# Optimization experiments

Hardware: AMD Instinct MI355X
Metric: run time of the kernel (lower is better)

Reference implementation:

```python
import jax, jax.numpy as jnp
import numpy as np

DIM = 768
NUM_HEADS = 12
HEAD_DIM = DIM // NUM_HEADS
SCALE = HEAD_DIM ** -0.5


def setup_inputs() -> dict:
    key = jax.random.key(0)
    ks = jax.random.split(key, 4)
    x = jax.random.normal(ks[0], (8, 1024, DIM), dtype=jnp.float32)
    # nn.Linear stores weight as [out, in]; we keep that convention.
    w_qkv = jax.random.normal(ks[1], (3 * DIM, DIM), dtype=jnp.float32) * (DIM ** -0.5)
    w_proj = jax.random.normal(ks[2], (DIM, DIM), dtype=jnp.float32) * (DIM ** -0.5)
    b_proj = jax.random.normal(ks[3], (DIM,), dtype=jnp.float32) * 0.02
    return {"x": x, "w_qkv": w_qkv, "w_proj": w_proj, "b_proj": b_proj}


def reference(x, w_qkv, w_proj, b_proj):
    B, N, C = x.shape
    H, D = NUM_HEADS, HEAD_DIM
    # qkv: [B, N, 3C] -> [3, B, H, N, D]
    qkv = jnp.einsum('bnc,oc->bno', x, w_qkv)
    qkv = qkv.reshape(B, N, 3, H, D).transpose(2, 0, 3, 1, 4)
    q, k, v = qkv[0] * SCALE, qkv[1], qkv[2]
    # attention scores [B, H, N, N]
    attn = jnp.einsum('bhnd,bhmd->bhnm', q, k)
    attn = jax.nn.softmax(attn, axis=-1)
    # weighted values -> [B, N, C]
    out = jnp.einsum('bhnm,bhmd->bhnd', attn, v)
    out = out.transpose(0, 2, 1, 3).reshape(B, N, C)
    # output projection
    return jnp.einsum('bnc,oc->bno', out, w_proj) + b_proj
```

## Files before the change

### kernel.cpp

```cpp
#include <hip/hip_runtime.h>
#include <hip/hip_bf16.h>
#include <math.h>


typedef unsigned short u16;
typedef __attribute__((ext_vector_type(8))) short bf16x8;
typedef __attribute__((ext_vector_type(4))) short bf16x4;
typedef __attribute__((ext_vector_type(4))) float f32x4;
typedef __attribute__((ext_vector_type(4))) unsigned int u32x4;

#define MFMA_BF16(a, b, c) __builtin_amdgcn_mfma_f32_16x16x32_bf16((a), (b), (c), 0, 0, 0)

#if __has_builtin(__builtin_amdgcn_mfma_f32_16x16x16bf16_1k)
#define MFMA16_BF16(a, b, c) __builtin_amdgcn_mfma_f32_16x16x16bf16_1k((a), (b), (c), 0, 0, 0)
#else
static __device__ __forceinline__ f32x4 MFMA16_BF16(bf16x4 a, bf16x4 b, f32x4 c) {
  f32x4 d;
  asm volatile("v_mfma_f32_16x16x16_bf16 %0, %1, %2, %3"
               : "=v"(d) : "v"(a), "v"(b), "v"(c));
  return d;
}
#endif

static __device__ __forceinline__ void gld_lds16(const void* g, void* l) {
  __builtin_amdgcn_global_load_lds(
      (__attribute__((address_space(1))) void*)(g),
      (__attribute__((address_space(3))) void*)(l), 16, 0, 0);
}

static __device__ __forceinline__ u16 f2bf(float f) {
  __hip_bfloat16 h = __float2bfloat16(f);
  return *(u16*)&h;
}

static __device__ __forceinline__ float fast_exp2(float x) {
#if __has_builtin(__builtin_amdgcn_exp2f)
  return __builtin_amdgcn_exp2f(x);
#else
  return exp2f(x);
#endif
}

static __device__ __forceinline__ void conv4(const float* src, u16* dst, int i) {
  const float4 v = *(const float4*)(src + i);
  float f0 = v.x, f1 = v.y, f2 = v.z, f3 = v.w;
  if (!isfinite(f0)) f0 = 0.f;
  if (!isfinite(f1)) f1 = 0.f;
  if (!isfinite(f2)) f2 = 0.f;
  if (!isfinite(f3)) f3 = 0.f;
  ushort4 o;
  o.x = f2bf(f0); o.y = f2bf(f1); o.z = f2bf(f2); o.w = f2bf(f3);
  *(ushort4*)(dst + i) = o;
}

__global__ __launch_bounds__(256) void convert3_kernel(
    const float* __restrict__ x,  u16* __restrict__ xb,
    const float* __restrict__ wq, u16* __restrict__ wqb,
    const float* __restrict__ wp, u16* __restrict__ wpb)
{
  const int blk = blockIdx.x;
  if (blk < 6144)      conv4(x,  xb,  (blk * 256 + threadIdx.x) * 4);
  else if (blk < 7872) conv4(wq, wqb, ((blk - 6144) * 256 + threadIdx.x) * 4);
  else                 conv4(wp, wpb, ((blk - 7872) * 256 + threadIdx.x) * 4);
}

__device__ __forceinline__ void gemm_tile_768(
    const u16* __restrict__ A, const u16* __restrict__ B,
    int m0, int n0, u16* ldsA, u16* ldsB, f32x4 acc[4][4])
{
  const int tid  = threadIdx.x;
  const int lane = tid & 63;
  const int wave = tid >> 6;
  const int quad = lane >> 4;
  const int l16  = lane & 15;
  const int wm = wave >> 1, wn = wave & 1;

  const u16* gA[4]; const u16* gB[4]; int ldsoff[4];
#pragma unroll
  for (int it = 0; it < 4; ++it) {
    const int c   = it * 256 + tid;
    const int row = c >> 3;
    const int cc  = (c & 7) ^ (row & 7);
    gA[it] = A + (size_t)(m0 + row) * 768 + cc * 8;
    gB[it] = B + (size_t)(n0 + row) * 768 + cc * 8;
    ldsoff[it] = (it * 256 + wave * 64) * 8;
  }

  for (int kt = 0; kt < 12; ++kt) {
    __syncthreads();
#pragma unroll
    for (int it = 0; it < 4; ++it) {
      gld_lds16(gA[it] + kt * 64, ldsA + ldsoff[it]);
      gld_lds16(gB[it] + kt * 64, ldsB + ldsoff[it]);
    }
    __syncthreads();
#pragma unroll
    for (int kc = 0; kc < 2; ++kc) {
      bf16x8 av[4], bv[4];
#pragma unroll
      for (int i = 0; i < 4; ++i) {
        const int rowA = wm * 64 + i * 16 + l16;
        av[i] = *(const bf16x8*)(ldsA + rowA * 64 + (((kc * 4 + quad) ^ (rowA & 7)) * 8));
        const int rowB = wn * 64 + i * 16 + l16;
        bv[i] = *(const bf16x8*)(ldsB + rowB * 64 + (((kc * 4 + quad) ^ (rowB & 7)) * 8));
      }
#pragma unroll
      for (int i = 0; i < 4; ++i)
#pragma unroll
        for (int j = 0; j < 4; ++j)
          acc[i][j] = MFMA_BF16(av[i], bv[j], acc[i][j]);
    }
  }
}


__global__ __launch_bounds__(256, 4) void qkv_gemm_kernel(
    const u16* __restrict__ X, const u16* __restrict__ W,
    u16* __restrict__ Qb, u16* __restrict__ Kb, u16* __restrict__ Vt)
{
  __shared__ alignas(16) u16 lds[2 * 128 * 64];
  u16* ldsA = lds;
  u16* ldsB = lds + 128 * 64;
  const int n0 = blockIdx.x * 128;
  const int m0 = blockIdx.y * 128;
  f32x4 acc[4][4];
  const f32x4 zero = {0.f, 0.f, 0.f, 0.f};
#pragma unroll
  for (int i = 0; i < 4; ++i)
#pragma unroll
    for (int j = 0; j < 4; ++j) acc[i][j] = zero;

  gemm_tile_768(X, W, m0, n0, ldsA, ldsB, acc);

  const int tid = threadIdx.x, lane = tid & 63, wave = tid >> 6;
  const int quad = lane >> 4, l16 = lane & 15;
  const int wm = wave >> 1, wn = wave & 1;

  const int which = blockIdx.x / 6;
  const bool isV = (which == 2);
  const float sc = (which == 0) ? 0.180336880f : 1.0f;
  u16* ep = lds;

  __syncthreads();
#pragma unroll
  for (int i = 0; i < 4; ++i)
#pragma unroll
    for (int j = 0; j < 4; ++j)
#pragma unroll
      for (int r = 0; r < 4; ++r) {
        const int m_l = wm * 64 + i * 16 + quad * 4 + r;
        const int o_l = wn * 64 + j * 16 + l16;
        const int row = isV ? o_l : m_l;
        const int col = isV ? m_l : o_l;
        const int ch  = col >> 3;
        const int chs = (ch & 8) | ((ch & 7) ^ (row & 7));
        ep[row * 128 + chs * 8 + (col & 7)] = f2bf(acc[i][j][r] * sc);
      }
  __syncthreads();

  const int row  = tid >> 1, half = tid & 1;
  const int b_   = m0 >> 10;
  const int nb   = m0 & 1023;
  const int oc0  = n0 - which * 768;
  u16* dst;
  if (!isV) {
    const int h = (oc0 >> 6) + half;
    dst = (which == 0 ? Qb : Kb) + (((size_t)(b_ * 12 + h)) * 1024 + nb + row) * 64;
  } else {
    const int h = (oc0 >> 6) + (row >> 6);
    const int d = row & 63;
    dst = Vt + (((size_t)(b_ * 12 + h)) * 64 + d) * 1024 + nb + half * 64;
  }
#pragma unroll
  for (int c = 0; c < 8; ++c) {
    const int chs = half * 8 + (c ^ (row & 7));
    *(u32x4*)(dst + c * 8) = *(const u32x4*)(ep + row * 128 + chs * 8);
  }
}

__global__ __launch_bounds__(256, 4) void proj_gemm_kernel(
    const u16* __restrict__ A, const u16* __restrict__ W,
    const float* __restrict__ bias, float* __restrict__ out)
{
  __shared__ alignas(16) u16 ldsA[128 * 64];
  __shared__ alignas(16) u16 ldsB[64 * 64];
  const int n0 = blockIdx.x * 64;
  const int m0 = blockIdx.y * 128;
  const int tid = threadIdx.x, lane = tid & 63, wave = tid >> 6;
  const int quad = lane >> 4, l16 = lane & 15;

  const u16* gA[4]; const u16* gB[2]; int loA[4], loB[2];
#pragma unroll
  for (int it = 0; it < 4; ++it) {
    const int c = it * 256 + tid, row = c >> 3, cc = (c & 7) ^ (row & 7);
    gA[it] = A + (size_t)(m0 + row) * 768 + cc * 8;
    loA[it] = (it * 256 + wave * 64) * 8;
  }
#pragma unroll
  for (int it = 0; it < 2; ++it) {
    const int c = it * 256 + tid, row = c >> 3, cc = (c & 7) ^ (row & 7);
    gB[it] = W + (size_t)(n0 + row) * 768 + cc * 8;
    loB[it] = (it * 256 + wave * 64) * 8;
  }

  f32x4 acc[2][4];
  const f32x4 zero = {0.f, 0.f, 0.f, 0.f};
#pragma unroll
  for (int s = 0; s < 2; ++s)
#pragma unroll
    for (int t = 0; t < 4; ++t) acc[s][t] = zero;

  for (int kt = 0; kt < 12; ++kt) {
    __syncthreads();
#pragma unroll
    for (int it = 0; it < 4; ++it) gld_lds16(gA[it] + kt * 64, ldsA + loA[it]);
#pragma unroll
    for (int it = 0; it < 2; ++it) gld_lds16(gB[it] + kt * 64, ldsB + loB[it]);
    __syncthreads();
#pragma unroll
    for (int kc = 0; kc < 2; ++kc) {
      bf16x8 av[2], bv[4];
#pragma unroll
      for (int s = 0; s < 2; ++s) {
        const int rowA = wave * 32 + s * 16 + l16;
        av[s] = *(const bf16x8*)(ldsA + rowA * 64 + (((kc * 4 + quad) ^ (rowA & 7)) * 8));
      }
#pragma unroll
      for (int t = 0; t < 4; ++t) {
        const int rowB = t * 16 + l16;
        bv[t] = *(const bf16x8*)(ldsB + rowB * 64 + (((kc * 4 + quad) ^ (rowB & 7)) * 8));
      }
#pragma unroll
      for (int s = 0; s < 2; ++s)
#pragma unroll
        for (int t = 0; t < 4; ++t)
          acc[s][t] = MFMA_BF16(av[s], bv[t], acc[s][t]);
    }
  }

  float bv4[4];
#pragma unroll
  for (int t = 0; t < 4; ++t) bv4[t] = bias[n0 + t * 16 + l16];
#pragma unroll
  for (int s = 0; s < 2; ++s)
#pragma unroll
    for (int t = 0; t < 4; ++t)
#pragma unroll
      for (int r = 0; r < 4; ++r) {
        const int m = m0 + wave * 32 + s * 16 + quad * 4 + r;
        out[(size_t)m * 768 + n0 + t * 16 + l16] = acc[s][t][r] + bv4[t];
      }
}

__global__ __launch_bounds__(256, 3) void attn_kernel(
    const u16* __restrict__ Q, const u16* __restrict__ K,
    const u16* __restrict__ Vt, __hip_bfloat16* __restrict__ O)
{
  __shared__ alignas(16) u16 ldsK[128 * 64];
  __shared__ alignas(16) u16 ldsV[64 * 128];
  const int bh = blockIdx.x;
  const int qb = blockIdx.y;
  const int tid = threadIdx.x;
  const int wave = tid >> 6, lane = tid & 63;
  const int quad = lane >> 4, l16 = lane & 15;

  const int q0 = qb * 128 + wave * 32;
  const u16* Kbh = K  + (size_t)bh * (1024 * 64);
  const u16* Vbh = Vt + (size_t)bh * (64 * 1024);

  const u16* gK[4]; const u16* gV[4]; int lo[4];
#pragma unroll
  for (int it = 0; it < 4; ++it) {
    const int c = it * 256 + tid;
    {
      const int row = c >> 3, cc = (c & 7) ^ (row & 7);
      gK[it] = Kbh + (size_t)row * 64 + cc * 8;
    }
    {
      const int row = c >> 4, slot = c & 15;
      const int cc = (slot & 8) | ((slot & 7) ^ (row & 7));
      gV[it] = Vbh + (size_t)row * 1024 + cc * 8;
    }
    lo[it] = (it * 256 + wave * 64) * 8;
  }

  bf16x8 aQ0[2], aQ1[2];
#pragma unroll
  for (int s = 0; s < 2; ++s) {
    const u16* qp = Q + ((size_t)bh * 1024 + q0 + s * 16 + l16) * 64 + quad * 8;
    aQ0[s] = *(const bf16x8*)qp;
    aQ1[s] = *(const bf16x8*)(qp + 32);
  }

  f32x4 oacc[2][4];
  const f32x4 zero = {0.f, 0.f, 0.f, 0.f};
#pragma unroll
  for (int s = 0; s < 2; ++s)
#pragma unroll
    for (int db = 0; db < 4; ++db) oacc[s][db] = zero;
  float lacc[2] = {0.f, 0.f};

  for (int kt = 0; kt < 8; ++kt) {
    __syncthreads();
#pragma unroll
    for (int it = 0; it < 4; ++it) {
      gld_lds16(gK[it] + (size_t)kt * 128 * 64, ldsK + lo[it]);
      gld_lds16(gV[it] + kt * 128, ldsV + lo[it]);
    }
    __syncthreads();

#pragma unroll
    for (int ph = 0; ph < 2; ++ph) {
      bf16x8 kb0[4], kb1[4];
#pragma unroll
      for (int t = 0; t < 4; ++t) {
        const int row = ph * 64 + t * 16 + l16;
        kb0[t] = *(const bf16x8*)(ldsK + row * 64 + (((0 * 4 + quad) ^ (row & 7)) * 8));
        kb1[t] = *(const bf16x8*)(ldsK + row * 64 + (((1 * 4 + quad) ^ (row & 7)) * 8));
      }
      bf16x4 pa[2][4];
#pragma unroll
      for (int s = 0; s < 2; ++s) {
#pragma unroll
        for (int t = 0; t < 4; ++t) {
          f32x4 z = zero;
          z = MFMA_BF16(kb0[t], aQ0[s], z);
          z = MFMA_BF16(kb1[t], aQ1[s], z);
          const float p0 = fast_exp2(z[0]);
          const float p1 = fast_exp2(z[1]);
          const float p2 = fast_exp2(z[2]);
          const float p3 = fast_exp2(z[3]);
          lacc[s] += (p0 + p1) + (p2 + p3);
          bf16x4 pk;
          pk[0] = (short)f2bf(p0); pk[1] = (short)f2bf(p1);
          pk[2] = (short)f2bf(p2); pk[3] = (short)f2bf(p3);
          pa[s][t] = pk;
        }
      }
#pragma unroll
      for (int db = 0; db < 4; ++db) {
        const int d = db * 16 + l16;
#pragma unroll
        for (int t = 0; t < 4; ++t) {
          const int slot = ph * 8 + ((t * 2 + (quad >> 1)) ^ (d & 7));
          const bf16x4 v = *(const bf16x4*)(ldsV + d * 128 + slot * 8 + (quad & 1) * 4);
#pragma unroll
          for (int s = 0; s < 2; ++s)
            oacc[s][db] = MFMA16_BF16(pa[s][t], v, oacc[s][db]);
        }
      }
    }
  }

  const int b = bh / 12, h = bh - (bh / 12) * 12;
  float linv[2];
#pragma unroll
  for (int s = 0; s < 2; ++s) {
    float l = lacc[s];
    l += __shfl_xor(l, 16);
    l += __shfl_xor(l, 32);
    linv[s] = 1.f / l;
  }
#pragma unroll
  for (int s = 0; s < 2; ++s) {
#pragma unroll
    for (int r = 0; r < 4; ++r) {
      const float inv = __shfl(linv[s], quad * 4 + r);
      const int n = q0 + s * 16 + quad * 4 + r;
      __hip_bfloat16* orow = O + ((size_t)b * 1024 + n) * 768 + h * 64;
#pragma unroll
      for (int db = 0; db < 4; ++db)
        orow[db * 16 + l16] = __float2bfloat16(oacc[s][db][r] * inv);
    }
  }
}

extern "C" void kernel_launch(void* const* d_in, const int* in_sizes, int n_in,
                              void* d_out, int out_size, void* d_ws, size_t ws_size,
                              hipStream_t stream) {
  const float* x      = (const float*)d_in[0];
  const float* w_qkv  = (const float*)d_in[1];
  const float* w_proj = (const float*)d_in[2];
  const float* b_proj = (const float*)d_in[3];
  float* out = (float*)d_out;

  char* ws = (char*)d_ws;
  const size_t SEG = (size_t)96 * 1024 * 64 * sizeof(u16);
  u16* xb   = (u16*)(ws + 0 * SEG);
  u16* Qb   = (u16*)(ws + 1 * SEG);
  u16* Kb   = (u16*)(ws + 2 * SEG);
  u16* AO   = (u16*)(ws + 3 * SEG);
  u16* Vt   = (u16*)(ws + 4 * SEG);
  u16* wqb  = (u16*)(ws + 5 * SEG);
  u16* wpb  = (u16*)(ws + 5 * SEG + 3538944);

  convert3_kernel<<<8448, 256, 0, stream>>>(x, xb, w_qkv, wqb, w_proj, wpb);
  qkv_gemm_kernel<<<dim3(18, 64), 256, 0, stream>>>(xb, wqb, Qb, Kb, Vt);
  attn_kernel    <<<dim3(96, 8), 256, 0, stream>>>(Qb, Kb, Vt, (__hip_bfloat16*)AO);
  proj_gemm_kernel<<<dim3(12, 64), 256, 0, stream>>>(AO, wpb, b_proj, out);
}
```

Measured before the change: 201.7 us.

## Split QKV GEMM and attention tiles across 8 waves per block

Both the QKV projection GEMM and the attention kernel now launch 512 threads (8 waves) per block while keeping the same tile sizes, so each wave owns half the previous work: a 64x32 sub-tile in the GEMM and 16 query rows in attention. Global-to-LDS loads are spread over more threads, and the QKV epilogue write-out is reindexed for four threads per row. The aim is more waves in flight to hide latency and lower register pressure per wave. In exchange, LDS fragment reuse per wave drops (K/V fragments are read from LDS twice as often relative to MFMA work), and synchronisation now covers more waves.

```diff
diff --git a/kernel.cpp b/kernel.cpp
--- a/kernel.cpp
+++ b/kernel.cpp
@@ -64,57 +64,8 @@
   else                 conv4(wp, wpb, ((blk - 7872) * 256 + threadIdx.x) * 4);
 }
 
-__device__ __forceinline__ void gemm_tile_768(
-    const u16* __restrict__ A, const u16* __restrict__ B,
-    int m0, int n0, u16* ldsA, u16* ldsB, f32x4 acc[4][4])
-{
-  const int tid  = threadIdx.x;
-  const int lane = tid & 63;
-  const int wave = tid >> 6;
-  const int quad = lane >> 4;
-  const int l16  = lane & 15;
-  const int wm = wave >> 1, wn = wave & 1;
-
-  const u16* gA[4]; const u16* gB[4]; int ldsoff[4];
-#pragma unroll
-  for (int it = 0; it < 4; ++it) {
-    const int c   = it * 256 + tid;
-    const int row = c >> 3;
-    const int cc  = (c & 7) ^ (row & 7);
-    gA[it] = A + (size_t)(m0 + row) * 768 + cc * 8;
-    gB[it] = B + (size_t)(n0 + row) * 768 + cc * 8;
-    ldsoff[it] = (it * 256 + wave * 64) * 8;
-  }
-
-  for (int kt = 0; kt < 12; ++kt) {
-    __syncthreads();
-#pragma unroll
-    for (int it = 0; it < 4; ++it) {
-      gld_lds16(gA[it] + kt * 64, ldsA + ldsoff[it]);
-      gld_lds16(gB[it] + kt * 64, ldsB + ldsoff[it]);
-    }
-    __syncthreads();
-#pragma unroll
-    for (int kc = 0; kc < 2; ++kc) {
-      bf16x8 av[4], bv[4];
-#pragma unroll
-      for (int i = 0; i < 4; ++i) {
-        const int rowA = wm * 64 + i * 16 + l16;
-        av[i] = *(const bf16x8*)(ldsA + rowA * 64 + (((kc * 4 + quad) ^ (rowA & 7)) * 8));
-        const int rowB = wn * 64 + i * 16 + l16;
-        bv[i] = *(const bf16x8*)(ldsB + rowB * 64 + (((kc * 4 + quad) ^ (rowB & 7)) * 8));
-      }
-#pragma unroll
-      for (int i = 0; i < 4; ++i)
-#pragma unroll
-        for (int j = 0; j < 4; ++j)
-          acc[i][j] = MFMA_BF16(av[i], bv[j], acc[i][j]);
-    }
-  }
-}
-
-
-__global__ __launch_bounds__(256, 4) void qkv_gemm_kernel(
+
+__global__ __launch_bounds__(512, 4) void qkv_gemm_kernel(
     const u16* __restrict__ X, const u16* __restrict__ W,
     u16* __restrict__ Qb, u16* __restrict__ Kb, u16* __restrict__ Vt)
 {
@@ -123,18 +74,56 @@
   u16* ldsB = lds + 128 * 64;
   const int n0 = blockIdx.x * 128;
   const int m0 = blockIdx.y * 128;
-  f32x4 acc[4][4];
-  const f32x4 zero = {0.f, 0.f, 0.f, 0.f};
-#pragma unroll
-  for (int i = 0; i < 4; ++i)
-#pragma unroll
-    for (int j = 0; j < 4; ++j) acc[i][j] = zero;
-
-  gemm_tile_768(X, W, m0, n0, ldsA, ldsB, acc);
-
   const int tid = threadIdx.x, lane = tid & 63, wave = tid >> 6;
   const int quad = lane >> 4, l16 = lane & 15;
-  const int wm = wave >> 1, wn = wave & 1;
+  const int wm = wave >> 2, wn = wave & 3;
+
+  const u16* gA[2]; const u16* gB[2]; int lo[2];
+#pragma unroll
+  for (int it = 0; it < 2; ++it) {
+    const int c = it * 512 + tid;
+    const int row = c >> 3;
+    const int cc  = (c & 7) ^ (row & 7);
+    gA[it] = X + (size_t)(m0 + row) * 768 + cc * 8;
+    gB[it] = W + (size_t)(n0 + row) * 768 + cc * 8;
+    lo[it] = (it * 512 + wave * 64) * 8;
+  }
+
+  f32x4 acc[4][2];
+  const f32x4 zero = {0.f, 0.f, 0.f, 0.f};
+#pragma unroll
+  for (int i = 0; i < 4; ++i)
+#pragma unroll
+    for (int j = 0; j < 2; ++j) acc[i][j] = zero;
+
+  for (int kt = 0; kt < 12; ++kt) {
+    __syncthreads();
+#pragma unroll
+    for (int it = 0; it < 2; ++it) {
+      gld_lds16(gA[it] + kt * 64, ldsA + lo[it]);
+      gld_lds16(gB[it] + kt * 64, ldsB + lo[it]);
+    }
+    __syncthreads();
+#pragma unroll
+    for (int kc = 0; kc < 2; ++kc) {
+      bf16x8 av[4], bv[2];
+#pragma unroll
+      for (int i = 0; i < 4; ++i) {
+        const int rowA = wm * 64 + i * 16 + l16;
+        av[i] = *(const bf16x8*)(ldsA + rowA * 64 + (((kc * 4 + quad) ^ (rowA & 7)) * 8));
+      }
+#pragma unroll
+      for (int j = 0; j < 2; ++j) {
+        const int rowB = wn * 32 + j * 16 + l16;
+        bv[j] = *(const bf16x8*)(ldsB + rowB * 64 + (((kc * 4 + quad) ^ (rowB & 7)) * 8));
+      }
+#pragma unroll
+      for (int i = 0; i < 4; ++i)
+#pragma unroll
+        for (int j = 0; j < 2; ++j)
+          acc[i][j] = MFMA_BF16(av[i], bv[j], acc[i][j]);
+    }
+  }
 
   const int which = blockIdx.x / 6;
   const bool isV = (which == 2);
@@ -145,11 +134,11 @@
 #pragma unroll
   for (int i = 0; i < 4; ++i)
 #pragma unroll
-    for (int j = 0; j < 4; ++j)
+    for (int j = 0; j < 2; ++j)
 #pragma unroll
       for (int r = 0; r < 4; ++r) {
         const int m_l = wm * 64 + i * 16 + quad * 4 + r;
-        const int o_l = wn * 64 + j * 16 + l16;
+        const int o_l = wn * 32 + j * 16 + l16;
         const int row = isV ? o_l : m_l;
         const int col = isV ? m_l : o_l;
         const int ch  = col >> 3;
@@ -158,23 +147,26 @@
       }
   __syncthreads();
 
-  const int row  = tid >> 1, half = tid & 1;
-  const int b_   = m0 >> 10;
-  const int nb   = m0 & 1023;
-  const int oc0  = n0 - which * 768;
-  u16* dst;
-  if (!isV) {
-    const int h = (oc0 >> 6) + half;
-    dst = (which == 0 ? Qb : Kb) + (((size_t)(b_ * 12 + h)) * 1024 + nb + row) * 64;
-  } else {
-    const int h = (oc0 >> 6) + (row >> 6);
-    const int d = row & 63;
-    dst = Vt + (((size_t)(b_ * 12 + h)) * 64 + d) * 1024 + nb + half * 64;
-  }
-#pragma unroll
-  for (int c = 0; c < 8; ++c) {
-    const int chs = half * 8 + (c ^ (row & 7));
-    *(u32x4*)(dst + c * 8) = *(const u32x4*)(ep + row * 128 + chs * 8);
+  const int row = tid >> 2, qtr = tid & 3;
+  const int b_  = m0 >> 10;
+  const int nb  = m0 & 1023;
+  const int oc0 = n0 - which * 768;
+#pragma unroll
+  for (int c = 0; c < 4; ++c) {
+    const int ch  = qtr * 4 + c;
+    const int chs = (ch & 8) | ((ch & 7) ^ (row & 7));
+    const u32x4 val = *(const u32x4*)(ep + row * 128 + chs * 8);
+    if (!isV) {
+      const int feat = ch * 8;
+      const int h = (oc0 >> 6) + (feat >> 6), d = feat & 63;
+      u16* dst = (which == 0 ? Qb : Kb) +
+                 (((size_t)(b_ * 12 + h)) * 1024 + nb + row) * 64 + d;
+      *(u32x4*)dst = val;
+    } else {
+      const int h = (oc0 >> 6) + (row >> 6), d = row & 63;
+      u16* dst = Vt + (((size_t)(b_ * 12 + h)) * 64 + d) * 1024 + nb + ch * 8;
+      *(u32x4*)dst = val;
+    }
   }
 }
 
@@ -252,7 +244,7 @@
       }
 }
 
-__global__ __launch_bounds__(256, 3) void attn_kernel(
+__global__ __launch_bounds__(512, 4) void attn_kernel(
     const u16* __restrict__ Q, const u16* __restrict__ K,
     const u16* __restrict__ Vt, __hip_bfloat16* __restrict__ O)
 {
@@ -264,14 +256,14 @@
   const int wave = tid >> 6, lane = tid & 63;
   const int quad = lane >> 4, l16 = lane & 15;
 
-  const int q0 = qb * 128 + wave * 32;
+  const int q0 = qb * 128 + wave * 16;
   const u16* Kbh = K  + (size_t)bh * (1024 * 64);
   const u16* Vbh = Vt + (size_t)bh * (64 * 1024);
 
-  const u16* gK[4]; const u16* gV[4]; int lo[4];
-#pragma unroll
-  for (int it = 0; it < 4; ++it) {
-    const int c = it * 256 + tid;
+  const u16* gK[2]; const u16* gV[2]; int lo[2];
+#pragma unroll
+  for (int it = 0; it < 2; ++it) {
+    const int c = it * 512 + tid;
     {
       const int row = c >> 3, cc = (c & 7) ^ (row & 7);
       gK[it] = Kbh + (size_t)row * 64 + cc * 8;
@@ -281,29 +273,23 @@
       const int cc = (slot & 8) | ((slot & 7) ^ (row & 7));
       gV[it] = Vbh + (size_t)row * 1024 + cc * 8;
     }
-    lo[it] = (it * 256 + wave * 64) * 8;
-  }
-
-  bf16x8 aQ0[2], aQ1[2];
-#pragma unroll
-  for (int s = 0; s < 2; ++s) {
-    const u16* qp = Q + ((size_t)bh * 1024 + q0 + s * 16 + l16) * 64 + quad * 8;
-    aQ0[s] = *(const bf16x8*)qp;
-    aQ1[s] = *(const bf16x8*)(qp + 32);
-  }
-
-  f32x4 oacc[2][4];
+    lo[it] = (it * 512 + wave * 64) * 8;
+  }
+
+  const u16* qp = Q + ((size_t)bh * 1024 + q0 + l16) * 64 + quad * 8;
+  const bf16x8 aQ0 = *(const bf16x8*)qp;
+  const bf16x8 aQ1 = *(const bf16x8*)(qp + 32);
+
+  f32x4 oacc[4];
   const f32x4 zero = {0.f, 0.f, 0.f, 0.f};
 #pragma unroll
-  for (int s = 0; s < 2; ++s)
-#pragma unroll
-    for (int db = 0; db < 4; ++db) oacc[s][db] = zero;
-  float lacc[2] = {0.f, 0.f};
+  for (int db = 0; db < 4; ++db) oacc[db] = zero;
+  float lacc = 0.f;
 
   for (int kt = 0; kt < 8; ++kt) {
     __syncthreads();
 #pragma unroll
-    for (int it = 0; it < 4; ++it) {
+    for (int it = 0; it < 2; ++it) {
       gld_lds16(gK[it] + (size_t)kt * 128 * 64, ldsK + lo[it]);
       gld_lds16(gV[it] + kt * 128, ldsV + lo[it]);
     }
@@ -318,24 +304,21 @@
         kb0[t] = *(const bf16x8*)(ldsK + row * 64 + (((0 * 4 + quad) ^ (row & 7)) * 8));
         kb1[t] = *(const bf16x8*)(ldsK + row * 64 + (((1 * 4 + quad) ^ (row & 7)) * 8));
       }
-      bf16x4 pa[2][4];
-#pragma unroll
-      for (int s = 0; s < 2; ++s) {
-#pragma unroll
-        for (int t = 0; t < 4; ++t) {
-          f32x4 z = zero;
-          z = MFMA_BF16(kb0[t], aQ0[s], z);
-          z = MFMA_BF16(kb1[t], aQ1[s], z);
-          const float p0 = fast_exp2(z[0]);
-          const float p1 = fast_exp2(z[1]);
-          const float p2 = fast_exp2(z[2]);
-          const float p3 = fast_exp2(z[3]);
-          lacc[s] += (p0 + p1) + (p2 + p3);
-          bf16x4 pk;
-          pk[0] = (short)f2bf(p0); pk[1] = (short)f2bf(p1);
-          pk[2] = (short)f2bf(p2); pk[3] = (short)f2bf(p3);
-          pa[s][t] = pk;
-        }
+      bf16x4 pa[4];
+#pragma unroll
+      for (int t = 0; t < 4; ++t) {
+        f32x4 z = zero;
+        z = MFMA_BF16(kb0[t], aQ0, z);
+        z = MFMA_BF16(kb1[t], aQ1, z);
+        const float p0 = fast_exp2(z[0]);
+        const float p1 = fast_exp2(z[1]);
+        const float p2 = fast_exp2(z[2]);
+        const float p3 = fast_exp2(z[3]);
+        lacc += (p0 + p1) + (p2 + p3);
+        bf16x4 pk;
+        pk[0] = (short)f2bf(p0); pk[1] = (short)f2bf(p1);
+        pk[2] = (short)f2bf(p2); pk[3] = (short)f2bf(p3);
+        pa[t] = pk;
       }
 #pragma unroll
       for (int db = 0; db < 4; ++db) {
@@ -344,34 +327,25 @@
         for (int t = 0; t < 4; ++t) {
           const int slot = ph * 8 + ((t * 2 + (quad >> 1)) ^ (d & 7));
           const bf16x4 v = *(const bf16x4*)(ldsV + d * 128 + slot * 8 + (quad & 1) * 4);
-#pragma unroll
-          for (int s = 0; s < 2; ++s)
-            oacc[s][db] = MFMA16_BF16(pa[s][t], v, oacc[s][db]);
+          oacc[db] = MFMA16_BF16(pa[t], v, oacc[db]);
         }
       }
     }
   }
 
   const int b = bh / 12, h = bh - (bh / 12) * 12;
-  float linv[2];
-#pragma unroll
-  for (int s = 0; s < 2; ++s) {
-    float l = lacc[s];
-    l += __shfl_xor(l, 16);
-    l += __shfl_xor(l, 32);
-    linv[s] = 1.f / l;
-  }
-#pragma unroll
-  for (int s = 0; s < 2; ++s) {
-#pragma unroll
-    for (int r = 0; r < 4; ++r) {
-      const float inv = __shfl(linv[s], quad * 4 + r);
-      const int n = q0 + s * 16 + quad * 4 + r;
-      __hip_bfloat16* orow = O + ((size_t)b * 1024 + n) * 768 + h * 64;
-#pragma unroll
-      for (int db = 0; db < 4; ++db)
-        orow[db * 16 + l16] = __float2bfloat16(oacc[s][db][r] * inv);
-    }
+  float l = lacc;
+  l += __shfl_xor(l, 16);
+  l += __shfl_xor(l, 32);
+  const float linv = 1.f / l;
+#pragma unroll
+  for (int r = 0; r < 4; ++r) {
+    const float inv = __shfl(linv, quad * 4 + r);
+    const int n = q0 + quad * 4 + r;
+    __hip_bfloat16* orow = O + ((size_t)b * 1024 + n) * 768 + h * 64;
+#pragma unroll
+    for (int db = 0; db < 4; ++db)
+      orow[db * 16 + l16] = __float2bfloat16(oacc[db][r] * inv);
   }
 }
 
@@ -395,7 +369,7 @@
   u16* wpb  = (u16*)(ws + 5 * SEG + 3538944);
 
   convert3_kernel<<<8448, 256, 0, stream>>>(x, xb, w_qkv, wqb, w_proj, wpb);
-  qkv_gemm_kernel<<<dim3(18, 64), 256, 0, stream>>>(xb, wqb, Qb, Kb, Vt);
-  attn_kernel    <<<dim3(96, 8), 256, 0, stream>>>(Qb, Kb, Vt, (__hip_bfloat16*)AO);
+  qkv_gemm_kernel<<<dim3(18, 64), 512, 0, stream>>>(xb, wqb, Qb, Kb, Vt);
+  attn_kernel    <<<dim3(96, 8), 512, 0, stream>>>(Qb, Kb, Vt, (__hip_bfloat16*)AO);
   proj_gemm_kernel<<<dim3(12, 64), 256, 0, stream>>>(AO, wpb, b_proj, out);
 }
```

Result: slower. 206.9 us (+2.6%).
